# Optimization experiments

Hardware: AMD Instinct MI355X
Metric: run time of the kernel (lower is better)

Reference implementation:

```python
import jax, jax.numpy as jnp
import numpy as np

B, QL, KL, D, H = 2, 2048, 2048, 1024, 16
E = D // H  # head dim


def setup_inputs() -> dict:
    key = jax.random.key(0)
    ks = jax.random.split(key, 12)
    query_features = jax.random.normal(ks[0], (B, QL, D), dtype=jnp.float32)
    key_features = jax.random.normal(ks[1], (B, KL, D), dtype=jnp.float32)
    # causal additive mask [QL, KL]: -inf above the diagonal, 0 elsewhere
    dependency_mask = jnp.where(
        jnp.arange(KL)[None, :] > jnp.arange(QL)[:, None], -jnp.inf, 0.0
    ).astype(jnp.float32)
    # key padding: random valid lengths in [KL//2, KL]; True = padded position
    lengths = jax.random.randint(ks[2], (B,), KL // 2, KL + 1)
    key_padding_mask = jnp.arange(KL)[None, :] >= lengths[:, None]
    s = 0.02
    Wq = jax.random.normal(ks[3], (D, D), jnp.float32) * s
    bq = jax.random.normal(ks[4], (D,), jnp.float32) * s
    Wk = jax.random.normal(ks[5], (D, D), jnp.float32) * s
    bk = jax.random.normal(ks[6], (D,), jnp.float32) * s
    Wv = jax.random.normal(ks[7], (D, D), jnp.float32) * s
    bv = jax.random.normal(ks[8], (D,), jnp.float32) * s
    Wo = jax.random.normal(ks[9], (D, D), jnp.float32) * s
    bo = jax.random.normal(ks[10], (D,), jnp.float32) * s
    return dict(query_features=query_features, key_features=key_features,
                dependency_mask=dependency_mask, key_padding_mask=key_padding_mask,
                Wq=Wq, bq=bq, Wk=Wk, bk=bk, Wv=Wv, bv=bv, Wo=Wo, bo=bo)


def reference(query_features, key_features, dependency_mask, key_padding_mask,
              Wq, bq, Wk, bk, Wv, bv, Wo, bo):
    b, kl, d = key_features.shape
    ql = query_features.shape[1]
    q = query_features @ Wq.T + bq          # [B, QL, D]
    k = key_features @ Wk.T + bk            # [B, KL, D]
    v = key_features @ Wv.T + bv            # [B, KL, D]
    qh = q.reshape(b, ql, H, E)
    kh = k.reshape(b, kl, H, E)
    vh = v.reshape(b, kl, H, E)
    # NOTE: original scales by sqrt(d_model), not sqrt(head_dim)
    scores = jnp.einsum('bqhe,bkhe->bhqk', qh, kh) / jnp.sqrt(jnp.float32(d))
    scores = jnp.where(key_padding_mask[:, None, None, :], -jnp.inf, scores)
    scores = scores + dependency_mask  # broadcast [QL,KL] over [B,H,QL,KL]
    probs = jax.nn.softmax(scores, axis=-1)  # dropout is identity in eval mode
    agg = jnp.einsum('bhqk,bkhe->bqhe', probs, vh).reshape(b, ql, d)
    return agg @ Wo.T + bo
```

## Files before the change

### kernel.cpp

```cpp
#include <hip/hip_runtime.h>
#include <hip/hip_bf16.h>


typedef __bf16 bf16x8 __attribute__((ext_vector_type(8)));
typedef float f32x4 __attribute__((ext_vector_type(4)));
typedef unsigned int u32x4 __attribute__((ext_vector_type(4)));
typedef unsigned short u16;
typedef unsigned int u32;

#define GLOBAL_AS __attribute__((address_space(1)))
#define LDS_AS __attribute__((address_space(3)))

static __device__ __forceinline__ u16 f2bf(float f) {
    __hip_bfloat16 h = __float2bfloat16(f);
    return __builtin_bit_cast(u16, h);
}
static __device__ __forceinline__ u32 pack2bf(float a, float b) {
    return (u32)f2bf(a) | ((u32)f2bf(b) << 16);
}
static __device__ __forceinline__ float exp2_hw(float x) {
    return __builtin_amdgcn_exp2f(x);
}

__global__ void cvt_all(const float* __restrict__ xq_f, const float* __restrict__ xk_f,
                        const float* __restrict__ wq_f, const float* __restrict__ wk_f,
                        const float* __restrict__ wv_f, const float* __restrict__ wo_f,
                        u16* __restrict__ xq, u16* __restrict__ xk,
                        u16* __restrict__ wq, u16* __restrict__ wk,
                        u16* __restrict__ wv, u16* __restrict__ wo,
                        const int* __restrict__ kpm, int* __restrict__ lens) {
    int blk = blockIdx.x;
    if (blk >= 12288) {
        const int b = blk - 12288, tid = threadIdx.x;
        int cnt = 0;
        #pragma unroll
        for (int i = 0; i < 8; ++i) cnt += (kpm[b * 2048 + i * 256 + tid] == 0) ? 1 : 0;
        #pragma unroll
        for (int off = 32; off; off >>= 1) cnt += __shfl_down(cnt, off);
        __shared__ int wsum[4];
        if ((tid & 63) == 0) wsum[tid >> 6] = cnt;
        __syncthreads();
        if (tid == 0) lens[b] = wsum[0] + wsum[1] + wsum[2] + wsum[3];
        return;
    }
    const float* s; u16* d; int i;
    if (blk < 4096)      { s = xq_f; d = xq; i = blk * 256 + threadIdx.x; }
    else if (blk < 8192) { s = xk_f; d = xk; i = (blk - 4096) * 256 + threadIdx.x; }
    else {
        int wsel = (blk - 8192) >> 10;
        i = ((blk - 8192) & 1023) * 256 + threadIdx.x;
        if (wsel == 0)      { s = wq_f; d = wq; }
        else if (wsel == 1) { s = wk_f; d = wk; }
        else if (wsel == 2) { s = wv_f; d = wv; }
        else                { s = wo_f; d = wo; }
    }
    float4 v = reinterpret_cast<const float4*>(s)[i];
    ushort4 o;
    o.x = f2bf(v.x); o.y = f2bf(v.y); o.z = f2bf(v.z); o.w = f2bf(v.w);
    reinterpret_cast<ushort4*>(d)[i] = o;
}

template<int OUT_F32, int BM, int BN>
__device__ __forceinline__
void gemm_body(const u16* __restrict__ A, const u16* __restrict__ Bw,
               const float* __restrict__ bias, void* __restrict__ Cout,
               int N, int K, float scale, int bx, int by) {
    constexpr int MREP = BM / 32, NREP = BN / 32;
    constexpr int ACH = BM / 8, TCH = ACH + BN / 8;
    constexpr int CPW = TCH / 4;
    __shared__ __attribute__((aligned(16))) u16 aS[BM * 64];
    __shared__ __attribute__((aligned(16))) u16 bS[BN * 64];
    const int tid = threadIdx.x, wave = tid >> 6, lane = tid & 63;
    const int m0 = by * BM, n0 = bx * BN;
    const int wr = wave >> 1, wc = wave & 1;
    const int fr = lane & 15, fq = lane >> 4;
    const int swz_col = (((lane & 7) ^ (lane >> 3)) * 8);
    const int rsw = (fr & 7) << 3;

    f32x4 acc[MREP][NREP] = {};

    for (int k0 = 0; k0 < K; k0 += 64) {
        #pragma unroll
        for (int i = 0; i < CPW; ++i) {
            int chunk = wave * CPW + i;
            const u16* gsrc; u16* ldst;
            if (chunk < ACH) {
                int row = chunk * 8 + (lane >> 3);
                gsrc = A + (size_t)(m0 + row) * K + k0 + swz_col;
                ldst = aS + chunk * 512;
            } else {
                int row = (chunk - ACH) * 8 + (lane >> 3);
                gsrc = Bw + (size_t)(n0 + row) * K + k0 + swz_col;
                ldst = bS + (chunk - ACH) * 512;
            }
            __builtin_amdgcn_global_load_lds((GLOBAL_AS void*)gsrc,
                                             (LDS_AS void*)ldst, 16, 0, 0);
        }
        __syncthreads();
        bf16x8 af[MREP][2], bfr[NREP][2];
        #pragma unroll
        for (int m = 0; m < MREP; ++m)
            #pragma unroll
            for (int h = 0; h < 2; ++h)
                af[m][h] = *reinterpret_cast<const bf16x8*>(
                    &aS[(wr * (BM / 2) + m * 16 + fr) * 64 + ((h * 32 + fq * 8) ^ rsw)]);
        #pragma unroll
        for (int n = 0; n < NREP; ++n)
            #pragma unroll
            for (int h = 0; h < 2; ++h)
                bfr[n][h] = *reinterpret_cast<const bf16x8*>(
                    &bS[(wc * (BN / 2) + n * 16 + fr) * 64 + ((h * 32 + fq * 8) ^ rsw)]);
        __builtin_amdgcn_s_setprio(1);
        #pragma unroll
        for (int m = 0; m < MREP; ++m)
            #pragma unroll
            for (int n = 0; n < NREP; ++n) {
                acc[m][n] = __builtin_amdgcn_mfma_f32_16x16x32_bf16(af[m][0], bfr[n][0], acc[m][n], 0, 0, 0);
                acc[m][n] = __builtin_amdgcn_mfma_f32_16x16x32_bf16(af[m][1], bfr[n][1], acc[m][n], 0, 0, 0);
            }
        __builtin_amdgcn_s_setprio(0);
        __syncthreads();
    }

    #pragma unroll
    for (int n = 0; n < NREP; ++n) {
        int col = n0 + wc * (BN / 2) + n * 16 + fr;
        float bv = bias[col];
        #pragma unroll
        for (int m = 0; m < MREP; ++m) {
            #pragma unroll
            for (int j = 0; j < 4; ++j) {
                int row = m0 + wr * (BM / 2) + m * 16 + fq * 4 + j;
                float v = (acc[m][n][j] + bv) * scale;
                if (OUT_F32)
                    reinterpret_cast<float*>(Cout)[(size_t)row * N + col] = v;
                else
                    reinterpret_cast<u16*>(Cout)[(size_t)row * N + col] = f2bf(v);
            }
        }
    }
}

__global__ __launch_bounds__(256, 3)
void gemm_qkv(const u16* __restrict__ xq, const u16* __restrict__ xk,
              const u16* __restrict__ wq, const u16* __restrict__ wk,
              const u16* __restrict__ wv,
              const float* __restrict__ bq, const float* __restrict__ bk,
              const float* __restrict__ bv,
              u16* __restrict__ qb, u16* __restrict__ kb, u16* __restrict__ vb) {
    const int id = blockIdx.x;
    const int g = id & 7, s = id >> 3;
    const int z = s >> 5;
    const int xl = (s >> 3) & 3, byl = s & 7;
    const int bx = (g & 1) * 4 + xl;
    const int by = (g >> 1) * 8 + byl;
    const u16* A = (z == 0) ? xq : xk;
    const u16* W = (z == 0) ? wq : (z == 1) ? wk : wv;
    const float* bias = (z == 0) ? bq : (z == 1) ? bk : bv;
    u16* C = (z == 0) ? qb : (z == 1) ? kb : vb;
    const float scale = (z == 0) ? 0.0450842200f : 1.0f;
    gemm_body<0, 128, 128>(A, W, bias, C, 1024, 1024, scale, bx, by);
}

__global__ __launch_bounds__(256, 2)
void gemm_out(const u16* __restrict__ A, const u16* __restrict__ Bw,
              const float* __restrict__ bias, float* __restrict__ Cout) {
    const int id = blockIdx.x;
    const int g = id & 7, s = id >> 3;
    const int xl = s & 3, byl = s >> 2;
    const int bx = (g & 1) * 4 + xl;
    const int by = (g >> 1) * 16 + byl;
    gemm_body<1, 64, 128>(A, Bw, bias, Cout, 1024, 1024, 1.0f, bx, by);
}

__global__ __launch_bounds__(256, 4)
void attn_fwd(const u16* __restrict__ Qb, const u16* __restrict__ Kb,
              const u16* __restrict__ Vb, const int* __restrict__ lens,
              u16* __restrict__ Ob) {
    __shared__ __attribute__((aligned(16))) u16 Ks[2][64 * 64];
    __shared__ __attribute__((aligned(16))) u16 Vts[2][64 * 64];
    const int tid = threadIdx.x, wave = tid >> 6, lane = tid & 63;
    const int id = blockIdx.x;
    const int bh = (id & 7) * 4 + ((id >> 3) & 3);
    const int k5 = id >> 5;
    const int g = k5 >> 3, x8 = k5 & 7;
    const int qt = (g == 0) ? x8 : (g == 1) ? 31 - x8 : (g == 2) ? 16 + x8 : 15 - x8;
    const int b = bh >> 4, h = bh & 15;
    const int q0 = qt * 64;
    const int fr = lane & 15, fq = lane >> 4;
    const int qrow = q0 + wave * 16;
    const int len = lens[b];
    const int nt = min(qt + 1, (len + 63) >> 6);

    const size_t qoff = (size_t)(b * 2048 + qrow + fr) * 1024 + h * 64 + fq * 8;
    bf16x8 qa0 = *reinterpret_cast<const bf16x8*>(Qb + qoff);
    bf16x8 qa1 = *reinterpret_cast<const bf16x8*>(Qb + qoff + 32);

    bf16x8 ones;
    #pragma unroll
    for (int i = 0; i < 8; ++i) ones[i] = __builtin_bit_cast(__bf16, (u16)0x3F80);

    f32x4 o_acc[4] = {};
    f32x4 lacc = {};

    const int e8 = tid >> 5;
    const int c2 = tid & 31;
    const int kp = 2 * c2;
    const int vhalf = kp >> 5, r5 = kp & 31;
    const int fqv = r5 >> 3, nv = (r5 >> 2) & 1, jv = r5 & 3;
    const int k_src = vhalf * 32 + nv * 16 + fqv * 4 + jv;
    const int kswz_col = (((lane & 7) ^ (lane >> 3)) * 8);

    auto issue_K = [&](int kt, int buf) {
        #pragma unroll
        for (int i = 0; i < 2; ++i) {
            int chunk = wave * 2 + i;
            int krow = chunk * 8 + (lane >> 3);
            const u16* gk = Kb + (size_t)(b * 2048 + kt * 64 + krow) * 1024 + h * 64 + kswz_col;
            __builtin_amdgcn_global_load_lds((GLOBAL_AS void*)gk,
                                             (LDS_AS void*)(&Ks[buf][chunk * 512]), 16, 0, 0);
        }
    };
    auto load_V = [&](int kt, ushort4* r) {
        const u16* b1 = Vb + (size_t)(b * 2048 + kt * 64 + k_src) * 1024 + h * 64 + e8 * 8;
        r[0] = reinterpret_cast<const ushort4*>(b1)[0];
        r[1] = reinterpret_cast<const ushort4*>(b1 + 4)[0];
        r[2] = reinterpret_cast<const ushort4*>(b1 + 1024)[0];
        r[3] = reinterpret_cast<const ushort4*>(b1 + 1024 + 4)[0];
    };
    auto write_V = [&](const ushort4* r, int buf) {
        u32* vbase = reinterpret_cast<u32*>(&Vts[buf][0]);
        const u16* lo16 = reinterpret_cast<const u16*>(&r[0]);
        const u16* hi16 = reinterpret_cast<const u16*>(&r[2]);
        #pragma unroll
        for (int i = 0; i < 8; ++i) {
            u32 w = (u32)lo16[i] | ((u32)hi16[i] << 16);
            vbase[(e8 * 8 + i) * 32 + (c2 ^ (i << 2))] = w;
        }
    };

    {
        ushort4 vr[4];
        issue_K(0, 0);
        load_V(0, vr);
        write_V(vr, 0);
    }
    __syncthreads();

    for (int kt = 0; kt < nt; ++kt) {
        const int k0 = kt * 64;
        const int cur = kt & 1, nxt = cur ^ 1;
        const bool has_next = (kt + 1 < nt);

        ushort4 vr[4];
        if (has_next) {
            issue_K(kt + 1, nxt);
            load_V(kt + 1, vr);
        }

        f32x4 s[4] = {};
        __builtin_amdgcn_s_setprio(1);
        #pragma unroll
        for (int n = 0; n < 4; ++n) {
            int kr = n * 16 + fr;
            int sw = (fr & 7) << 3;
            bf16x8 kb0 = *reinterpret_cast<const bf16x8*>(&Ks[cur][kr * 64 + ((fq * 8) ^ sw)]);
            bf16x8 kb1 = *reinterpret_cast<const bf16x8*>(&Ks[cur][kr * 64 + ((32 + fq * 8) ^ sw)]);
            s[n] = __builtin_amdgcn_mfma_f32_16x16x32_bf16(kb0, qa0, s[n], 0, 0, 0);
            s[n] = __builtin_amdgcn_mfma_f32_16x16x32_bf16(kb1, qa1, s[n], 0, 0, 0);
        }
        __builtin_amdgcn_s_setprio(0);

        const bool fullt = (k0 + 63 <= qrow) && (k0 + 64 <= len);
        if (!fullt) {
            const int qg = qrow + fr;
            #pragma unroll
            for (int n = 0; n < 4; ++n)
                #pragma unroll
                for (int j = 0; j < 4; ++j) {
                    int kg = k0 + n * 16 + fq * 4 + j;
                    s[n][j] = (kg <= qg && kg < len) ? s[n][j] : -1e30f;
                }
        }
        #pragma unroll
        for (int n = 0; n < 4; ++n)
            #pragma unroll
            for (int j = 0; j < 4; ++j)
                s[n][j] = exp2_hw(s[n][j]);

        u32x4 w0, w1;
        w0[0] = pack2bf(s[0][0], s[0][1]); w0[1] = pack2bf(s[0][2], s[0][3]);
        w0[2] = pack2bf(s[1][0], s[1][1]); w0[3] = pack2bf(s[1][2], s[1][3]);
        w1[0] = pack2bf(s[2][0], s[2][1]); w1[1] = pack2bf(s[2][2], s[2][3]);
        w1[2] = pack2bf(s[3][0], s[3][1]); w1[3] = pack2bf(s[3][2], s[3][3]);
        bf16x8 pa0 = __builtin_bit_cast(bf16x8, w0);
        bf16x8 pa1 = __builtin_bit_cast(bf16x8, w1);

        __builtin_amdgcn_s_setprio(1);
        lacc = __builtin_amdgcn_mfma_f32_16x16x32_bf16(pa0, ones, lacc, 0, 0, 0);
        #pragma unroll
        for (int n = 0; n < 4; ++n) {
            int vr2 = n * 16 + fr;
            bf16x8 vb2 = *reinterpret_cast<const bf16x8*>(
                &Vts[cur][vr2 * 64 + ((fq * 8) ^ ((fr & 7) << 3))]);
            o_acc[n] = __builtin_amdgcn_mfma_f32_16x16x32_bf16(pa0, vb2, o_acc[n], 0, 0, 0);
        }
        lacc = __builtin_amdgcn_mfma_f32_16x16x32_bf16(pa1, ones, lacc, 0, 0, 0);
        #pragma unroll
        for (int n = 0; n < 4; ++n) {
            int vr2 = n * 16 + fr;
            bf16x8 vb2 = *reinterpret_cast<const bf16x8*>(
                &Vts[cur][vr2 * 64 + ((32 + fq * 8) ^ ((fr & 7) << 3))]);
            o_acc[n] = __builtin_amdgcn_mfma_f32_16x16x32_bf16(pa1, vb2, o_acc[n], 0, 0, 0);
        }
        __builtin_amdgcn_s_setprio(0);

        if (has_next) write_V(vr, nxt);
        __syncthreads();
    }

    #pragma unroll
    for (int j = 0; j < 4; ++j) {
        float inv = 1.f / lacc[j];
        int row = qrow + fq * 4 + j;
        #pragma unroll
        for (int n = 0; n < 4; ++n) {
            int col = h * 64 + n * 16 + fr;
            Ob[(size_t)(b * 2048 + row) * 1024 + col] = f2bf(o_acc[n][j] * inv);
        }
    }
}

extern "C" void kernel_launch(void* const* d_in, const int* in_sizes, int n_in,
                              void* d_out, int out_size, void* d_ws, size_t ws_size,
                              hipStream_t stream) {
    const float* xq_f = (const float*)d_in[0];
    const float* xk_f = (const float*)d_in[1];
    const int* kpm = (const int*)d_in[3];
    const float* Wq = (const float*)d_in[4];
    const float* bq = (const float*)d_in[5];
    const float* Wk = (const float*)d_in[6];
    const float* bk = (const float*)d_in[7];
    const float* Wv = (const float*)d_in[8];
    const float* bv = (const float*)d_in[9];
    const float* Wo = (const float*)d_in[10];
    const float* bo = (const float*)d_in[11];

    u16* ws = (u16*)d_ws;
    u16* xq = ws;
    u16* xk = xq + 4194304;
    u16* wq = xk + 4194304;
    u16* wk = wq + 1048576;
    u16* wv = wk + 1048576;
    u16* wo = wv + 1048576;
    u16* qb = wo + 1048576;
    u16* kb2 = qb + 4194304;
    u16* vb2 = kb2 + 4194304;
    u16* ag = vb2 + 4194304;
    int* lens = (int*)(ag + 4194304);

    cvt_all<<<12290, 256, 0, stream>>>(xq_f, xk_f, Wq, Wk, Wv, Wo,
                                       xq, xk, wq, wk, wv, wo, kpm, lens);

    gemm_qkv<<<768, 256, 0, stream>>>(xq, xk, wq, wk, wv,
                                      bq, bk, bv, qb, kb2, vb2);

    attn_fwd<<<1024, 256, 0, stream>>>(qb, kb2, vb2, lens, ag);

    gemm_out<<<512, 256, 0, stream>>>(ag, wo, bo, (float*)d_out);
}
```

Measured before the change: 101.6 us.

## Split long causal query tiles across two KV halves and combine partials

For the upper half of query tiles (the longest causal rows), each tile is split into two blocks that each process half of the key tiles and write unnormalized fp32 partial outputs and row sums to scratch. A new combine kernel sums the two partials and normalizes to bf16. The aim is better load balance and more blocks, so long tiles stop dominating the attention tail. The cost is an extra kernel launch and extra global traffic for the partials, and launch bounds rise to 5 waves per SIMD. The combine relies on the kernel not subtracting a running max, so partial sums can be added directly.

```diff
diff --git a/kernel.cpp b/kernel.cpp
--- a/kernel.cpp
+++ b/kernel.cpp
@@ -173,24 +173,34 @@
     gemm_body<1, 64, 128>(A, Bw, bias, Cout, 1024, 1024, 1.0f, bx, by);
 }
 
-__global__ __launch_bounds__(256, 4)
+__global__ __launch_bounds__(256, 5)
 void attn_fwd(const u16* __restrict__ Qb, const u16* __restrict__ Kb,
               const u16* __restrict__ Vb, const int* __restrict__ lens,
-              u16* __restrict__ Ob) {
+              u16* __restrict__ Ob, float* __restrict__ Opart,
+              float* __restrict__ Lpart) {
     __shared__ __attribute__((aligned(16))) u16 Ks[2][64 * 64];
     __shared__ __attribute__((aligned(16))) u16 Vts[2][64 * 64];
     const int tid = threadIdx.x, wave = tid >> 6, lane = tid & 63;
     const int id = blockIdx.x;
     const int bh = (id & 7) * 4 + ((id >> 3) & 3);
     const int k5 = id >> 5;
-    const int g = k5 >> 3, x8 = k5 & 7;
-    const int qt = (g == 0) ? x8 : (g == 1) ? 31 - x8 : (g == 2) ? 16 + x8 : 15 - x8;
     const int b = bh >> 4, h = bh & 15;
-    const int q0 = qt * 64;
+    const int len = lens[b];
+    const int L64 = (len + 63) >> 6;
+    int qt, kt0, ktE, khalf, pair; bool split;
+    if (k5 < 32) {
+        qt = 31 - (k5 >> 1); khalf = k5 & 1; split = true;
+        int ntf = min(qt + 1, L64);
+        int mid = ntf >> 1;
+        kt0 = khalf ? mid : 0;
+        ktE = khalf ? ntf : mid;
+        pair = (bh << 4) + (qt - 16);
+    } else {
+        qt = 47 - k5; khalf = 0; split = false; pair = 0;
+        kt0 = 0; ktE = min(qt + 1, L64);
+    }
     const int fr = lane & 15, fq = lane >> 4;
-    const int qrow = q0 + wave * 16;
-    const int len = lens[b];
-    const int nt = min(qt + 1, (len + 63) >> 6);
+    const int qrow = qt * 64 + wave * 16;
 
     const size_t qoff = (size_t)(b * 2048 + qrow + fr) * 1024 + h * 64 + fq * 8;
     bf16x8 qa0 = *reinterpret_cast<const bf16x8*>(Qb + qoff);
@@ -241,16 +251,16 @@
 
     {
         ushort4 vr[4];
-        issue_K(0, 0);
-        load_V(0, vr);
+        issue_K(kt0, 0);
+        load_V(kt0, vr);
         write_V(vr, 0);
     }
     __syncthreads();
 
-    for (int kt = 0; kt < nt; ++kt) {
+    for (int kt = kt0; kt < ktE; ++kt) {
         const int k0 = kt * 64;
-        const int cur = kt & 1, nxt = cur ^ 1;
-        const bool has_next = (kt + 1 < nt);
+        const int cur = (kt - kt0) & 1, nxt = cur ^ 1;
+        const bool has_next = (kt + 1 < ktE);
 
         ushort4 vr[4];
         if (has_next) {
@@ -319,15 +329,56 @@
         __syncthreads();
     }
 
+    if (!split) {
+        #pragma unroll
+        for (int j = 0; j < 4; ++j) {
+            float inv = 1.f / lacc[j];
+            int row = qrow + fq * 4 + j;
+            #pragma unroll
+            for (int n = 0; n < 4; ++n) {
+                int col = h * 64 + n * 16 + fr;
+                Ob[(size_t)(b * 2048 + row) * 1024 + col] = f2bf(o_acc[n][j] * inv);
+            }
+        }
+    } else {
+        float* Op = Opart + (size_t)(khalf * 512 + pair) * 4096;
+        float* Lp = Lpart + (khalf * 512 + pair) * 64;
+        #pragma unroll
+        for (int j = 0; j < 4; ++j) {
+            int ql = wave * 16 + fq * 4 + j;
+            #pragma unroll
+            for (int n = 0; n < 4; ++n)
+                Op[ql * 64 + n * 16 + fr] = o_acc[n][j];
+            if (fr == 0) Lp[ql] = lacc[j];
+        }
+    }
+}
+
+__global__ __launch_bounds__(256, 8)
+void attn_combine(const float* __restrict__ Opart, const float* __restrict__ Lpart,
+                  u16* __restrict__ Ob) {
+    const int p = blockIdx.x;
+    const int tid = threadIdx.x;
+    const int bh = p >> 4, t = p & 15;
+    const int b = bh >> 4, h = bh & 15;
+    const int qt = 16 + t;
+    const int r = tid >> 2, c0 = (tid & 3) * 16;
+    const float la = Lpart[p * 64 + r];
+    const float lb = Lpart[(512 + p) * 64 + r];
+    const float inv = 1.f / (la + lb);
+    const float* A = Opart + (size_t)p * 4096 + r * 64 + c0;
+    const float* Bp = Opart + (size_t)(512 + p) * 4096 + r * 64 + c0;
+    u16* dst = Ob + (size_t)(b * 2048 + qt * 64 + r) * 1024 + h * 64 + c0;
     #pragma unroll
-    for (int j = 0; j < 4; ++j) {
-        float inv = 1.f / lacc[j];
-        int row = qrow + fq * 4 + j;
-        #pragma unroll
-        for (int n = 0; n < 4; ++n) {
-            int col = h * 64 + n * 16 + fr;
-            Ob[(size_t)(b * 2048 + row) * 1024 + col] = f2bf(o_acc[n][j] * inv);
-        }
+    for (int i = 0; i < 4; ++i) {
+        float4 a = reinterpret_cast<const float4*>(A)[i];
+        float4 bb = reinterpret_cast<const float4*>(Bp)[i];
+        ushort4 o;
+        o.x = f2bf((a.x + bb.x) * inv);
+        o.y = f2bf((a.y + bb.y) * inv);
+        o.z = f2bf((a.z + bb.z) * inv);
+        o.w = f2bf((a.w + bb.w) * inv);
+        reinterpret_cast<ushort4*>(dst)[i] = o;
     }
 }
 
@@ -359,13 +410,18 @@
     u16* ag = vb2 + 4194304;
     int* lens = (int*)(ag + 4194304);
 
+    float* Opart = (float*)xq;
+    float* Lpart = (float*)wq;
+
     cvt_all<<<12290, 256, 0, stream>>>(xq_f, xk_f, Wq, Wk, Wv, Wo,
                                        xq, xk, wq, wk, wv, wo, kpm, lens);
 
     gemm_qkv<<<768, 256, 0, stream>>>(xq, xk, wq, wk, wv,
                                       bq, bk, bv, qb, kb2, vb2);
 
-    attn_fwd<<<1024, 256, 0, stream>>>(qb, kb2, vb2, lens, ag);
+    attn_fwd<<<1536, 256, 0, stream>>>(qb, kb2, vb2, lens, ag, Opart, Lpart);
+
+    attn_combine<<<512, 256, 0, stream>>>(Opart, Lpart, ag);
 
     gemm_out<<<512, 256, 0, stream>>>(ag, wo, bo, (float*)d_out);
 }
```

Result: slower. 111.9 us (+10.2%).
